# Optimization experiments

Hardware: AMD Instinct MI355X
Metric: run time of the kernel (lower is better)

The kernel has to match this reference:

```python
import jax, jax.numpy as jnp
import numpy as np

B, N, D = 2, 2048, 1536
HEADS, KVH, DQK, DV = 8, 1, 128, 192
G = HEADS // KVH  # query groups per kv head
NP, DP = 512, 128  # pairwise seq len (coarse), pairwise feature dim
SCALE = DQK ** -0.5
CLAMP = 5.0
MOMENTUM = 0.1  # BatchRMSNorm: 1 - 0.9
EPS = 1e-5


def layernorm(x, w, b):
    mu = jnp.mean(x, axis=-1, keepdims=True)
    var = jnp.mean(jnp.square(x - mu), axis=-1, keepdims=True)
    return (x - mu) * jax.lax.rsqrt(var + EPS) * w + b


def setup_inputs() -> dict:
    key = jax.random.key(0)
    ks = jax.random.split(key, 6)
    w = lambda k, shape: jax.random.normal(k, shape, jnp.float32) * 0.02
    return {
        "x": jax.random.normal(ks[0], (B, N, D), jnp.float32),
        "pairwise": jax.random.normal(ks[1], (B, NP, NP, DP), jnp.float32),
        "w_qkv": w(ks[2], (D, HEADS * DQK + KVH * DQK + KVH * DV)),
        "q_w": jnp.ones((DQK,), jnp.float32), "q_b": jnp.zeros((DQK,), jnp.float32),
        "k_w": jnp.ones((DQK,), jnp.float32), "k_b": jnp.zeros((DQK,), jnp.float32),
        "v_w": jnp.ones((DV,), jnp.float32), "v_b": jnp.zeros((DV,), jnp.float32),
        "bias_gamma": jnp.ones((DP,), jnp.float32),
        "bias_beta": jnp.zeros((DP,), jnp.float32),
        "bias_running_var": jnp.ones((DP,), jnp.float32),
        "w_bias": w(ks[3], (DP, HEADS)),
        "w_out": w(ks[4], (HEADS * DV, D)),
        "b_out": jnp.zeros((D,), jnp.float32),
    }


def reference(x, pairwise, w_qkv, q_w, q_b, k_w, k_b, v_w, v_b,
              bias_gamma, bias_beta, bias_running_var, w_bias, w_out, b_out):
    b, n, _ = x.shape
    qkv = x @ w_qkv
    q, k, v = jnp.split(qkv, [HEADS * DQK, HEADS * DQK + KVH * DQK], axis=-1)
    # split heads: q -> b g h n d, k/v -> b h n d
    q = q.reshape(b, n, G, KVH, DQK).transpose(0, 2, 3, 1, 4)
    k = k.reshape(b, n, KVH, DQK).transpose(0, 2, 1, 3)
    v = v.reshape(b, n, KVH, DV).transpose(0, 2, 1, 3)
    q = layernorm(q, q_w, q_b)
    k = layernorm(k, k_w, k_b)
    v = layernorm(v, v_w, v_b)

    sim = jnp.einsum('bghid,bhjd->bghij', q, k) * SCALE

    # BatchRMSNorm (training update of running_var, then normalize)
    flat = pairwise.reshape(-1, DP)
    batch_var = jnp.var(flat, axis=0)  # unbiased=False
    rv = bias_running_var * (1.0 - MOMENTUM) + MOMENTUM * batch_var
    std = jnp.sqrt(rv + EPS)
    normed = pairwise / std * bias_gamma + bias_beta
    bias = jax.nn.gelu(normed, approximate=False) @ w_bias  # b i j (g h)
    bias = bias.reshape(b, NP, NP, G, KVH).transpose(0, 3, 4, 1, 2)  # b g h i j
    r = n // NP  # expand_factor
    bias = jnp.repeat(jnp.repeat(bias, r, axis=-2), r, axis=-1)

    sim = jnp.tanh((sim + bias) / CLAMP) * CLAMP  # softclamp
    attn = jax.nn.softmax(sim, axis=-1)
    out = jnp.einsum('bghij,bhjd->bghid', attn, v)
    out = out.transpose(0, 3, 1, 2, 4).reshape(b, n, HEADS * DV)  # merge heads
    return out @ w_out + b_out
```

## Files before the change

kernel.cpp:

```cpp
#include <hip/hip_runtime.h>
#include <math.h>

typedef _Float16 f16;
typedef unsigned int u32;
typedef __attribute__((ext_vector_type(8))) f16 f16x8;
typedef __attribute__((ext_vector_type(4))) f16 f16x4;
typedef __attribute__((ext_vector_type(4))) float f32x4;
typedef __attribute__((ext_vector_type(16))) float f32x16;

#define DEV static __device__ __forceinline__

#define NB 2
#define SEQ 2048
#define DMODEL 1536
#define NHEADS 8
#define DQK 128
#define DVV 192
#define QKVW 1344
#define SCALEQK 0.08838834764831845f
#define LOG2E 1.4426950408889634f

#define OFF_WQKVT 0ull
#define OFF_WOUTT 4128768ull
#define OFF_QKV   8847360ull
#define OFF_Q     30867456ull
#define OFF_K     39256064ull
#define OFF_V     40304640ull
#define OFF_VT    41877504ull
#define OFF_VSUM  43450368ull
#define OFF_SG    43451392ull
#define OFF_BIASC 43452416ull
#define OFF_AO    60229632ull

DEV float fexp2(float x){
#if __has_builtin(__builtin_amdgcn_exp2f)
  return __builtin_amdgcn_exp2f(x);
#else
  return exp2f(x);
#endif
}
DEV float frcp(float x){
#if __has_builtin(__builtin_amdgcn_rcpf)
  return __builtin_amdgcn_rcpf(x);
#else
  return 1.0f/x;
#endif
}

typedef u32 __attribute__((address_space(1))) u32g;
typedef u32 __attribute__((address_space(3))) u32l;
DEV void g2l16(const void* g, void* l){
  __builtin_amdgcn_global_load_lds((const u32g*)g, (u32l*)l, 16, 0, 0);
}

#define MFMA32(a,b,c) __builtin_amdgcn_mfma_f32_32x32x16_f16(a,b,c,0,0,0)
#define MFMA16(a,b,c) __builtin_amdgcn_mfma_f32_16x16x32_f16(a,b,c,0,0,0)

DEV f32x16 zero16(){
  f32x16 v;
  #pragma unroll
  for (int i=0;i<16;i++) v[i]=0.f;
  return v;
}
DEV f32x4 zero4(){
  f32x4 v;
  #pragma unroll
  for (int i=0;i<4;i++) v[i]=0.f;
  return v;
}
DEV float gelu_f(float x){ return 0.5f*x*(1.f + erff(x*0.70710678118654752440f)); }

__global__ void wtrans(const float* __restrict__ src, f16* __restrict__ dst, int K, int N){
  __shared__ float t[32][33];
  int k0 = blockIdx.x*32, n0 = blockIdx.y*32;
  int tx = threadIdx.x, ty = threadIdx.y;
  #pragma unroll
  for (int i=0;i<4;i++){ int r = ty+8*i; t[r][tx] = src[(size_t)(k0+r)*N + n0+tx]; }
  __syncthreads();
  #pragma unroll
  for (int i=0;i<4;i++){ int r = ty+8*i; dst[(size_t)(n0+r)*K + k0+tx] = (f16)t[tx][r]; }
}

__global__ __launch_bounds__(256,2) void qkv_gemm(const float* __restrict__ X,
                                                  const f16* __restrict__ WT,
                                                  float* __restrict__ qkv){
  __shared__ char lds[49152];
  int nb = blockIdx.x*64, mb = blockIdx.y*128;
  int tid = threadIdx.x;
  int w = tid>>6, lane = tid&63, li = lane&31, h = lane>>5;
  int arow = tid>>4, acq = tid&15;
  int brow = lane>>3, bc = lane&7;
  f32x16 acc[2]; acc[0]=zero16(); acc[1]=zero16();
  f32x4 ar[8];

#define QG_ISSUE_B(buf, kt_) do { \
    char* bd = lds + (buf)*24576 + 16384; \
    _Pragma("unroll") \
    for (int s=0;s<2;s++){ \
      int slot = w*2+s; int nl = slot*8 + brow; int cs = bc ^ (nl&7); \
      g2l16(WT + (size_t)(nb+nl)*DMODEL + (kt_)*64 + cs*8, bd + slot*1024); \
    } } while(0)
#define QG_LOAD_A(kt_) do { \
    _Pragma("unroll") \
    for (int i=0;i<8;i++) \
      ar[i] = *(const f32x4*)(X + (size_t)(mb + arow + 16*i)*DMODEL + (kt_)*64 + acq*4); \
    } while(0)
#define QG_WRITE_A(buf) do { \
    char* ad = lds + (buf)*24576; \
    _Pragma("unroll") \
    for (int i=0;i<8;i++){ \
      int rr = arow + 16*i; int ch = (acq>>1) ^ (rr&7); \
      f16x4 t4; t4[0]=(f16)ar[i][0]; t4[1]=(f16)ar[i][1]; t4[2]=(f16)ar[i][2]; t4[3]=(f16)ar[i][3]; \
      *(f16x4*)(ad + rr*128 + ch*16 + (acq&1)*8) = t4; \
    } } while(0)

  QG_ISSUE_B(0,0); QG_LOAD_A(0); QG_WRITE_A(0);
  __syncthreads();
  for (int kt=0; kt<24; kt++){
    int cur = kt&1;
    if (kt<23){ QG_ISSUE_B(cur^1, kt+1); QG_LOAD_A(kt+1); }
    const char* ad = lds + cur*24576;
    const char* bd = lds + cur*24576 + 16384;
    int ml = w*32 + li;
    #pragma unroll
    for (int ks=0; ks<4; ks++){
      f16x8 af = *(const f16x8*)(ad + ml*128 + (((2*ks+h) ^ (ml&7))*16));
      #pragma unroll
      for (int nf=0; nf<2; nf++){
        int nl = nf*32 + li;
        f16x8 bf = *(const f16x8*)(bd + nl*128 + (((2*ks+h) ^ (nl&7))*16));
        acc[nf] = MFMA32(af, bf, acc[nf]);
      }
    }
    if (kt<23) QG_WRITE_A(cur^1);
    __syncthreads();
  }
  #pragma unroll
  for (int nf=0; nf<2; nf++)
    #pragma unroll
    for (int r=0;r<16;r++){
      int m = mb + w*32 + (r&3) + 8*(r>>2) + 4*h;
      int n = nb + nf*32 + li;
      qkv[(size_t)m*QKVW + n] = acc[nf][r];
    }
#undef QG_ISSUE_B
#undef QG_LOAD_A
#undef QG_WRITE_A
}

__global__ __launch_bounds__(64) void ln_pack(const float* __restrict__ qkv,
    const float* __restrict__ qw, const float* __restrict__ qb,
    const float* __restrict__ kw, const float* __restrict__ kb,
    const float* __restrict__ vw, const float* __restrict__ vb,
    f16* __restrict__ Q, f16* __restrict__ K, f16* __restrict__ V){
  int bid = blockIdx.x;
  int row = bid / 10, seg = bid - row*10;
  int b = row >> 11, n = row & 2047;
  int lane = threadIdx.x;
  const float* base = qkv + (size_t)row*QKVW;
  if (seg < 9){
    int off = seg*128;
    float x0 = base[off+lane], x1 = base[off+64+lane];
    float s = x0+x1;
    #pragma unroll
    for (int d=32; d>=1; d>>=1) s += __shfl_xor(s, d);
    float mu = s*(1.f/128.f);
    float d0 = x0-mu, d1 = x1-mu;
    float vv = d0*d0 + d1*d1;
    #pragma unroll
    for (int d=32; d>=1; d>>=1) vv += __shfl_xor(vv, d);
    float istd = rsqrtf(vv*(1.f/128.f) + 1e-5f);
    const float* W  = (seg<8)? qw : kw;
    const float* Bi = (seg<8)? qb : kb;
    f16* dst = (seg<8) ? (Q + ((size_t)(b*NHEADS+seg)*SEQ + n)*DQK)
                       : (K + ((size_t)(b*SEQ+n))*DQK);
    dst[lane]    = (f16)(d0*istd*W[lane] + Bi[lane]);
    dst[lane+64] = (f16)(d1*istd*W[lane+64] + Bi[lane+64]);
  } else {
    float x0 = base[1152+lane], x1 = base[1152+64+lane], x2 = base[1152+128+lane];
    float s = x0+x1+x2;
    #pragma unroll
    for (int d=32; d>=1; d>>=1) s += __shfl_xor(s, d);
    float mu = s*(1.f/192.f);
    float d0=x0-mu, d1=x1-mu, d2=x2-mu;
    float vv = d0*d0+d1*d1+d2*d2;
    #pragma unroll
    for (int d=32; d>=1; d>>=1) vv += __shfl_xor(vv, d);
    float istd = rsqrtf(vv*(1.f/192.f) + 1e-5f);
    f16* dst = V + (size_t)(b*SEQ+n)*DVV;
    dst[lane]     = (f16)(d0*istd*vw[lane] + vb[lane]);
    dst[lane+64]  = (f16)(d1*istd*vw[lane+64] + vb[lane+64]);
    dst[lane+128] = (f16)(d2*istd*vw[lane+128] + vb[lane+128]);
  }
}

__global__ void vtrans(const f16* __restrict__ V, f16* __restrict__ VT){
  __shared__ f16 t[32][33];
  int b = blockIdx.z; int d0 = blockIdx.x*32; int j0 = blockIdx.y*32;
  int tx = threadIdx.x, ty = threadIdx.y;
  #pragma unroll
  for (int i=0;i<4;i++){ int r = ty+8*i; t[r][tx] = V[((size_t)b*SEQ + j0+r)*DVV + d0+tx]; }
  __syncthreads();
  #pragma unroll
  for (int i=0;i<4;i++){ int r = ty+8*i; VT[((size_t)b*DVV + d0+r)*SEQ + j0+tx] = t[tx][r]; }
}

__global__ __launch_bounds__(256,4) void pvar(const float* __restrict__ pw, float* __restrict__ sums){
  int tid = threadIdx.x;
  int c = tid & 127, hh = tid >> 7;
  float s1 = 0.f, s2 = 0.f;
  const float* p0 = pw + ((size_t)blockIdx.x*512 + hh)*128 + c;
  #pragma unroll 4
  for (int it=0; it<256; it++){
    float v = p0[(size_t)it*256];
    s1 += v; s2 += v*v;
  }
  __shared__ float r1[256], r2[256];
  r1[tid] = s1; r2[tid] = s2;
  __syncthreads();
  if (tid < 128){
    atomicAdd(&sums[c],     r1[tid] + r1[tid+128]);
    atomicAdd(&sums[128+c], r2[tid] + r2[tid+128]);
  }
}

__global__ void finvar(const float* __restrict__ sums, const float* __restrict__ rvar,
                       const float* __restrict__ gamma, const float* __restrict__ beta,
                       float* __restrict__ sg, float* __restrict__ sb){
  int c = threadIdx.x;
  const float Minv = 1.f/524288.f;
  float m = sums[c]*Minv;
  float var = sums[128+c]*Minv - m*m;
  float rv = rvar[c]*0.9f + 0.1f*var;
  float istd = rsqrtf(rv + 1e-5f);
  sg[c] = istd*gamma[c];
  sb[c] = beta[c];
}

__global__ __launch_bounds__(256,2) void bias_gemm(const float* __restrict__ pw,
    const float* __restrict__ sg, const float* __restrict__ sb,
    const float* __restrict__ wb, float* __restrict__ biasc){
  int tid = threadIdx.x;
  int w = tid>>6, lane = tid&63;
  int il = lane&15, kg = lane>>4;
  f16x8 bw[4];
  float sgr[32], sbr[32];
  #pragma unroll
  for (int t=0;t<4;t++)
    #pragma unroll
    for (int e=0;e<8;e++){
      int k = t*32 + kg*8 + e;
      bw[t][e] = (f16)((il<8) ? wb[k*8 + il] : 0.f);
      sgr[t*8+e] = sg[k];
      sbr[t*8+e] = sb[k];
    }
  for (int it=0; it<8; it++){
    int tile = blockIdx.x*4 + w + it*4096;
    size_t rg = (size_t)tile*16 + il;
    f32x4 acc = zero4();
    #pragma unroll
    for (int t=0;t<4;t++){
      const float* sp = pw + rg*128 + t*32 + kg*8;
      f32x4 v0 = *(const f32x4*)sp;
      f32x4 v1 = *(const f32x4*)(sp+4);
      f16x8 af;
      #pragma unroll
      for (int e=0;e<4;e++) af[e]   = (f16)gelu_f(v0[e]*sgr[t*8+e]   + sbr[t*8+e]);
      #pragma unroll
      for (int e=0;e<4;e++) af[4+e] = (f16)gelu_f(v1[e]*sgr[t*8+4+e] + sbr[t*8+4+e]);
      acc = MFMA16(af, bw[t], acc);
    }
    if (il < 8){
      #pragma unroll
      for (int r=0;r<4;r++){
        size_t rr = (size_t)tile*16 + kg*4 + r;
        int bb = (int)(rr >> 18);
        int rem = (int)(rr & 262143);
        int ii = rem >> 9, jj = rem & 511;
        biasc[(((size_t)(bb*8 + il)*512) + ii)*512 + jj] = acc[r];
      }
    }
  }
}

__global__ __launch_bounds__(256,1) void attn(const f16* __restrict__ Q, const f16* __restrict__ K,
                                              const f16* __restrict__ VT, const float* __restrict__ biasc,
                                              f16* __restrict__ AO){
  __shared__ char lds[81920];
  __shared__ float linvb[4][32];
  int bid = blockIdx.x;
  int bg = bid & 15, qt = bid >> 4;
  int b = bg >> 3, g = bg & 7;
  int tid = threadIdx.x;
  int w = tid >> 6, lane = tid & 63;
  int li = lane & 31, h = lane >> 5;

  const f16* Qb = Q  + (size_t)bg*SEQ*DQK;
  const f16* Kb = K  + (size_t)b*SEQ*DQK;
  const f16* Vb = VT + (size_t)b*DVV*SEQ;

  int qrow = qt*128 + w*32 + li;
  f16x8 qf[8];
  #pragma unroll
  for (int ks=0; ks<8; ks++)
    qf[ks] = *(const f16x8*)(Qb + (size_t)qrow*DQK + ks*16 + h*8);

  const float* brow = biasc + ((size_t)bg*512 + (qrow>>2))*512;

  f32x16 oacc[6];
  #pragma unroll
  for (int nf=0;nf<6;nf++) oacc[nf] = zero16();
  float lsum = 0.f;

  int kl_row = lane >> 4, kl_c = lane & 15;
  int vl_row = lane >> 3, vl_c = lane & 7;

#define STAGE(buf, jt_) do { \
    char* kd = lds + (buf)*40960; \
    const f16* ksrc = Kb + (size_t)(jt_)*64*DQK; \
    _Pragma("unroll") \
    for (int s=0;s<4;s++){ \
      int slot = w*4+s; int jr = slot*4 + kl_row; int cs = kl_c ^ (jr&7); \
      g2l16(ksrc + (size_t)jr*DQK + cs*8, kd + slot*1024); \
    } \
    char* vd = lds + (buf)*40960 + 16384; \
    _Pragma("unroll") \
    for (int s=0;s<6;s++){ \
      int slot = w*6+s; int dvr = slot*8 + vl_row; int cs = vl_c ^ (dvr&7); \
      g2l16(Vb + (size_t)dvr*SEQ + (size_t)(jt_)*64 + cs*8, vd + slot*1024); \
    } } while(0)

  STAGE(0, 0);

  const float CS = SCALEQK * (2.f*LOG2E/5.f);
  const float CB = 2.f*LOG2E/5.f;
  const float CP = 5.f*LOG2E;

  for (int jt=0; jt<32; jt++){
    int cur = jt & 1;
    __syncthreads();
    if (jt < 31) STAGE(cur^1, jt+1);
    const char* kb_ = lds + cur*40960;
    const char* vb_ = lds + cur*40960 + 16384;
    #pragma unroll
    for (int sub=0; sub<2; sub++){
      f32x16 sacc = zero16();
      int jr = sub*32 + li;
      #pragma unroll
      for (int ks=0; ks<8; ks++){
        int ck = (2*ks + h) ^ (jr&7);
        f16x8 kf = *(const f16x8*)(kb_ + jr*256 + ck*16);
        sacc = MFMA32(kf, qf[ks], sacc);
      }
      int jb4 = jt*16 + sub*8;
      float bt[4];
      #pragma unroll
      for (int q=0;q<4;q++) bt[q] = brow[jb4 + 2*q + h] * CB;
      float p[16], xp[16];
      #pragma unroll
      for (int r=0;r<16;r++){
        float u2 = sacc[r]*CS + bt[r>>2];
        float E  = fexp2(u2);
        float tn = 1.f - 2.f*frcp(E + 1.f);
        float pr = fexp2(tn * CP);
        p[r] = pr;
        lsum += pr;
      }
      #pragma unroll
      for (int r=0;r<16;r++) xp[r] = __shfl_xor(p[r], 32);
      #pragma unroll
      for (int ks2=0; ks2<2; ks2++){
        f16x8 pa;
        #pragma unroll
        for (int e=0;e<4;e++) pa[e] = (f16)(h ? xp[8*ks2+4+e] : p[8*ks2+e]);
        #pragma unroll
        for (int e=4;e<8;e++) pa[e] = (f16)(h ? p[8*ks2+e]    : xp[8*ks2+e-4]);
        #pragma unroll
        for (int nf=0; nf<6; nf++){
          int dvr = nf*32 + li;
          int cj = (sub*4 + 2*ks2 + h) ^ (dvr&7);
          f16x8 vf = *(const f16x8*)(vb_ + dvr*128 + cj*16);
          oacc[nf] = MFMA32(pa, vf, oacc[nf]);
        }
      }
    }
  }
  float ltot = lsum + __shfl_xor(lsum, 32);
  float linv = 1.f / ltot;
  if (h == 0) linvb[w][li] = linv;
  __syncthreads();
  #pragma unroll
  for (int nf=0; nf<6; nf++)
    #pragma unroll
    for (int r=0;r<16;r++){
      int il = (r&3) + 8*(r>>2) + 4*h;
      float ov = oacc[nf][r] * linvb[w][il];
      int orow = qt*128 + w*32 + il;
      AO[((size_t)(b*SEQ + orow)*NHEADS + g)*DVV + nf*32 + li] = (f16)ov;
    }
#undef STAGE
}

__global__ __launch_bounds__(256,2) void out_gemm(const f16* __restrict__ A, const f16* __restrict__ WT,
                                                  const float* __restrict__ bo, float* __restrict__ out){
  __shared__ char lds[49152];
  int nb = blockIdx.x*64, mb = blockIdx.y*128;
  int tid = threadIdx.x;
  int w = tid>>6, lane = tid&63, li = lane&31, h = lane>>5;
  int srow = lane>>3, sc = lane&7;
  f32x16 acc[2]; acc[0]=zero16(); acc[1]=zero16();

#define OG_STAGE(buf, kt_) do { \
    char* ad = lds + (buf)*24576; \
    _Pragma("unroll") \
    for (int s=0;s<4;s++){ \
      int slot = w*4+s; int mlr = slot*8 + srow; int cs = sc ^ (mlr&7); \
      g2l16(A + (size_t)(mb+mlr)*DMODEL + (kt_)*64 + cs*8, ad + slot*1024); \
    } \
    char* bd = lds + (buf)*24576 + 16384; \
    _Pragma("unroll") \
    for (int s=0;s<2;s++){ \
      int slot = w*2+s; int nl = slot*8 + srow; int cs = sc ^ (nl&7); \
      g2l16(WT + (size_t)(nb+nl)*DMODEL + (kt_)*64 + cs*8, bd + slot*1024); \
    } } while(0)

  OG_STAGE(0,0);
  __syncthreads();
  for (int kt=0; kt<24; kt++){
    int cur = kt&1;
    if (kt<23) OG_STAGE(cur^1, kt+1);
    const char* ad = lds + cur*24576;
    const char* bd = lds + cur*24576 + 16384;
    int ml = w*32 + li;
    #pragma unroll
    for (int ks=0; ks<4; ks++){
      f16x8 af = *(const f16x8*)(ad + ml*128 + (((2*ks+h) ^ (ml&7))*16));
      #pragma unroll
      for (int nf=0; nf<2; nf++){
        int nl = nf*32 + li;
        f16x8 bf = *(const f16x8*)(bd + nl*128 + (((2*ks+h) ^ (nl&7))*16));
        acc[nf] = MFMA32(af, bf, acc[nf]);
      }
    }
    __syncthreads();
  }
  float bo0 = bo[nb+li], bo1 = bo[nb+32+li];
  #pragma unroll
  for (int nf=0; nf<2; nf++)
    #pragma unroll
    for (int r=0;r<16;r++){
      int m = mb + w*32 + (r&3) + 8*(r>>2) + 4*h;
      int n = nb + nf*32 + li;
      out[(size_t)m*DMODEL + n] = acc[nf][r] + (nf ? bo1 : bo0);
    }
#undef OG_STAGE
}

extern "C" void kernel_launch(void* const* d_in, const int* in_sizes, int n_in,
                              void* d_out, int out_size, void* d_ws, size_t ws_size,
                              hipStream_t stream) {
  (void)in_sizes; (void)n_in; (void)out_size; (void)ws_size;
  const float* x        = (const float*)d_in[0];
  const float* pairwise = (const float*)d_in[1];
  const float* w_qkv    = (const float*)d_in[2];
  const float* q_w      = (const float*)d_in[3];
  const float* q_b      = (const float*)d_in[4];
  const float* k_w      = (const float*)d_in[5];
  const float* k_b      = (const float*)d_in[6];
  const float* v_w      = (const float*)d_in[7];
  const float* v_b      = (const float*)d_in[8];
  const float* bgamma   = (const float*)d_in[9];
  const float* bbeta    = (const float*)d_in[10];
  const float* brvar    = (const float*)d_in[11];
  const float* w_bias   = (const float*)d_in[12];
  const float* w_out    = (const float*)d_in[13];
  const float* b_out    = (const float*)d_in[14];
  float* out = (float*)d_out;

  char* ws = (char*)d_ws;
  f16*   wqkvT = (f16*)(ws + OFF_WQKVT);
  f16*   woutT = (f16*)(ws + OFF_WOUTT);
  float* qkvb  = (float*)(ws + OFF_QKV);
  f16*   Qh    = (f16*)(ws + OFF_Q);
  f16*   Kh    = (f16*)(ws + OFF_K);
  f16*   Vh    = (f16*)(ws + OFF_V);
  f16*   VTh   = (f16*)(ws + OFF_VT);
  float* vsum  = (float*)(ws + OFF_VSUM);
  float* sg    = (float*)(ws + OFF_SG);
  float* sb    = sg + 128;
  float* biasc = (float*)(ws + OFF_BIASC);
  f16*   AOh   = (f16*)(ws + OFF_AO);

  (void)hipMemsetAsync(ws + OFF_VSUM, 0, 1024, stream);
  wtrans<<<dim3(48,42), dim3(32,8), 0, stream>>>(w_qkv, wqkvT, 1536, 1344);
  wtrans<<<dim3(48,48), dim3(32,8), 0, stream>>>(w_out, woutT, 1536, 1536);
  qkv_gemm<<<dim3(21,32), 256, 0, stream>>>(x, wqkvT, qkvb);
  ln_pack<<<40960, 64, 0, stream>>>(qkvb, q_w,q_b,k_w,k_b,v_w,v_b, Qh, Kh, Vh);
  vtrans<<<dim3(6,64,2), dim3(32,8), 0, stream>>>(Vh, VTh);
  pvar<<<1024, 256, 0, stream>>>(pairwise, vsum);
  finvar<<<1, 128, 0, stream>>>(vsum, brvar, bgamma, bbeta, sg, sb);
  bias_gemm<<<1024, 256, 0, stream>>>(pairwise, sg, sb, w_bias, biasc);
  attn<<<256, 256, 0, stream>>>(Qh, Kh, VTh, biasc, AOh);
  out_gemm<<<dim3(24,32), 256, 0, stream>>>(AOh, woutT, b_out, out);
}
```

Before: 350.3 us.

## Merge preprocessing kernels into four launches, store bias in fp16, tune attention

Cuts the launch count by combining the two weight transposes into one launch and interleaving the QKV GEMM with the pairwise variance reduction in a single grid. The variance now uses per-block partials instead of atomics, so the memset goes away. LayerNorm is merged with the variance finalisation, and the bias GEMM with the V transpose. The coarse bias is stored as fp16 to halve its traffic in attention. Attention also raises wave priority around its MFMA sections and passes the softmax normaliser by lane shuffle instead of LDS plus a barrier. Risks are lower bias precision, load imbalance in the mixed grids, and possible under-occupancy of the mixed blocks.

```diff
diff --git a/kernel.cpp b/kernel.cpp
--- a/kernel.cpp
+++ b/kernel.cpp
@@ -10,7 +10,6 @@
 
 #define DEV static __device__ __forceinline__
 
-#define NB 2
 #define SEQ 2048
 #define DMODEL 1536
 #define NHEADS 8
@@ -27,10 +26,10 @@
 #define OFF_K     39256064ull
 #define OFF_V     40304640ull
 #define OFF_VT    41877504ull
-#define OFF_VSUM  43450368ull
-#define OFF_SG    43451392ull
-#define OFF_BIASC 43452416ull
-#define OFF_AO    60229632ull
+#define OFF_PART  43450368ull
+#define OFF_SG    43712512ull
+#define OFF_BIASC 43713536ull
+#define OFF_AO    52102144ull
 
 DEV float fexp2(float x){
 #if __has_builtin(__builtin_amdgcn_exp2f)
@@ -70,23 +69,25 @@
 }
 DEV float gelu_f(float x){ return 0.5f*x*(1.f + erff(x*0.70710678118654752440f)); }
 
-__global__ void wtrans(const float* __restrict__ src, f16* __restrict__ dst, int K, int N){
+__global__ __launch_bounds__(256) void k1_wtrans(const float* __restrict__ wq, f16* __restrict__ wqT,
+                                                 const float* __restrict__ wo, f16* __restrict__ woT){
   __shared__ float t[32][33];
-  int k0 = blockIdx.x*32, n0 = blockIdx.y*32;
-  int tx = threadIdx.x, ty = threadIdx.y;
+  int bid = blockIdx.x, tid = threadIdx.x;
+  int tx = tid & 31, ty = tid >> 5;
+  const float* src; f16* dst; int N, x, y;
+  if (bid < 2016){ src = wq; dst = wqT; N = 1344; x = bid % 48; y = bid / 48; }
+  else { int b2 = bid - 2016; src = wo; dst = woT; N = 1536; x = b2 % 48; y = b2 / 48; }
+  int k0 = x*32, n0 = y*32;
   #pragma unroll
   for (int i=0;i<4;i++){ int r = ty+8*i; t[r][tx] = src[(size_t)(k0+r)*N + n0+tx]; }
   __syncthreads();
   #pragma unroll
-  for (int i=0;i<4;i++){ int r = ty+8*i; dst[(size_t)(n0+r)*K + k0+tx] = (f16)t[tx][r]; }
-}
-
-__global__ __launch_bounds__(256,2) void qkv_gemm(const float* __restrict__ X,
-                                                  const f16* __restrict__ WT,
-                                                  float* __restrict__ qkv){
-  __shared__ char lds[49152];
-  int nb = blockIdx.x*64, mb = blockIdx.y*128;
-  int tid = threadIdx.x;
+  for (int i=0;i<4;i++){ int r = ty+8*i; dst[(size_t)(n0+r)*1536 + k0+tx] = (f16)t[tx][r]; }
+}
+
+DEV void qkv_body(const float* __restrict__ X, const f16* __restrict__ WT,
+                  float* __restrict__ qkv, char* lds, int bx, int by, int tid){
+  int nb = bx*64, mb = by*128;
   int w = tid>>6, lane = tid&63, li = lane&31, h = lane>>5;
   int arow = tid>>4, acq = tid&15;
   int brow = lane>>3, bc = lane&7;
@@ -148,15 +149,47 @@
 #undef QG_WRITE_A
 }
 
-__global__ __launch_bounds__(64) void ln_pack(const float* __restrict__ qkv,
+DEV void pvar_body(const float* __restrict__ pw, float* __restrict__ partials,
+                   char* smem, int id, int tid){
+  int c = tid & 127, hh = tid >> 7;
+  float s1 = 0.f, s2 = 0.f;
+  const float* p0 = pw + ((size_t)id*2048 + hh)*128 + c;
+  #pragma unroll 8
+  for (int it=0; it<1024; it++){
+    float v = p0[(size_t)it*256];
+    s1 += v; s2 += v*v;
+  }
+  float* r1 = (float*)smem; float* r2 = r1 + 256;
+  r1[tid] = s1; r2[tid] = s2;
+  __syncthreads();
+  if (tid < 128){
+    partials[(size_t)id*256 + tid]       = r1[tid] + r1[tid+128];
+    partials[(size_t)id*256 + 128 + tid] = r2[tid] + r2[tid+128];
+  }
+}
+
+__global__ __launch_bounds__(256,2) void k2_qkv_pvar(const float* __restrict__ X,
+    const f16* __restrict__ WT, float* __restrict__ qkv,
+    const float* __restrict__ pw, float* __restrict__ partials){
+  __shared__ char smem[49152];
+  int bid = blockIdx.x, tid = threadIdx.x;
+  if (bid < 512){
+    if ((bid & 1) == 0){ int qid = bid>>1; qkv_body(X, WT, qkv, smem, qid%21, qid/21, tid); }
+    else               { pvar_body(pw, partials, smem, bid>>1, tid); }
+  } else {
+    int qid = 256 + (bid - 512);
+    qkv_body(X, WT, qkv, smem, qid%21, qid/21, tid);
+  }
+}
+
+DEV void ln_unit(const float* __restrict__ qkv,
     const float* __restrict__ qw, const float* __restrict__ qb,
     const float* __restrict__ kw, const float* __restrict__ kb,
     const float* __restrict__ vw, const float* __restrict__ vb,
-    f16* __restrict__ Q, f16* __restrict__ K, f16* __restrict__ V){
-  int bid = blockIdx.x;
-  int row = bid / 10, seg = bid - row*10;
+    f16* __restrict__ Q, f16* __restrict__ K, f16* __restrict__ V,
+    int unit, int lane){
+  int row = unit / 10, seg = unit - row*10;
   int b = row >> 11, n = row & 2047;
-  int lane = threadIdx.x;
   const float* base = qkv + (size_t)row*QKVW;
   if (seg < 9){
     int off = seg*128;
@@ -194,53 +227,40 @@
   }
 }
 
-__global__ void vtrans(const f16* __restrict__ V, f16* __restrict__ VT){
-  __shared__ f16 t[32][33];
-  int b = blockIdx.z; int d0 = blockIdx.x*32; int j0 = blockIdx.y*32;
-  int tx = threadIdx.x, ty = threadIdx.y;
-  #pragma unroll
-  for (int i=0;i<4;i++){ int r = ty+8*i; t[r][tx] = V[((size_t)b*SEQ + j0+r)*DVV + d0+tx]; }
-  __syncthreads();
-  #pragma unroll
-  for (int i=0;i<4;i++){ int r = ty+8*i; VT[((size_t)b*DVV + d0+r)*SEQ + j0+tx] = t[tx][r]; }
-}
-
-__global__ __launch_bounds__(256,4) void pvar(const float* __restrict__ pw, float* __restrict__ sums){
-  int tid = threadIdx.x;
-  int c = tid & 127, hh = tid >> 7;
-  float s1 = 0.f, s2 = 0.f;
-  const float* p0 = pw + ((size_t)blockIdx.x*512 + hh)*128 + c;
-  #pragma unroll 4
-  for (int it=0; it<256; it++){
-    float v = p0[(size_t)it*256];
-    s1 += v; s2 += v*v;
-  }
-  __shared__ float r1[256], r2[256];
-  r1[tid] = s1; r2[tid] = s2;
-  __syncthreads();
-  if (tid < 128){
-    atomicAdd(&sums[c],     r1[tid] + r1[tid+128]);
-    atomicAdd(&sums[128+c], r2[tid] + r2[tid+128]);
-  }
-}
-
-__global__ void finvar(const float* __restrict__ sums, const float* __restrict__ rvar,
-                       const float* __restrict__ gamma, const float* __restrict__ beta,
-                       float* __restrict__ sg, float* __restrict__ sb){
-  int c = threadIdx.x;
-  const float Minv = 1.f/524288.f;
-  float m = sums[c]*Minv;
-  float var = sums[128+c]*Minv - m*m;
-  float rv = rvar[c]*0.9f + 0.1f*var;
-  float istd = rsqrtf(rv + 1e-5f);
-  sg[c] = istd*gamma[c];
-  sb[c] = beta[c];
-}
-
-__global__ __launch_bounds__(256,2) void bias_gemm(const float* __restrict__ pw,
+__global__ __launch_bounds__(256,4) void k3_ln_finvar(const float* __restrict__ qkv,
+    const float* __restrict__ qw, const float* __restrict__ qb,
+    const float* __restrict__ kw, const float* __restrict__ kb,
+    const float* __restrict__ vw, const float* __restrict__ vb,
+    f16* __restrict__ Q, f16* __restrict__ K, f16* __restrict__ V,
+    const float* __restrict__ partials, const float* __restrict__ rvar,
+    const float* __restrict__ gamma, const float* __restrict__ beta,
+    float* __restrict__ sg, float* __restrict__ sb){
+  __shared__ float sh[256];
+  int bid = blockIdx.x, tid = threadIdx.x;
+  if (bid < 10240){
+    ln_unit(qkv, qw,qb,kw,kb,vw,vb, Q,K,V, bid*4 + (tid>>6), tid&63);
+  } else {
+    int c = tid & 127, wh = tid >> 7;
+    float acc = 0.f;
+    #pragma unroll 4
+    for (int i=0;i<256;i++) acc += partials[i*256 + wh*128 + c];
+    sh[tid] = acc;
+    __syncthreads();
+    if (tid < 128){
+      float s1 = sh[tid], s2 = sh[tid+128];
+      const float Minv = 1.f/524288.f;
+      float m = s1*Minv;
+      float var = s2*Minv - m*m;
+      float rv = rvar[tid]*0.9f + 0.1f*var;
+      sg[tid] = rsqrtf(rv + 1e-5f)*gamma[tid];
+      sb[tid] = beta[tid];
+    }
+  }
+}
+
+DEV void bias_body(const float* __restrict__ pw,
     const float* __restrict__ sg, const float* __restrict__ sb,
-    const float* __restrict__ wb, float* __restrict__ biasc){
-  int tid = threadIdx.x;
+    const float* __restrict__ wb, f16* __restrict__ biasc, int bias_id, int tid){
   int w = tid>>6, lane = tid&63;
   int il = lane&15, kg = lane>>4;
   f16x8 bw[4];
@@ -255,7 +275,7 @@
       sbr[t*8+e] = sb[k];
     }
   for (int it=0; it<8; it++){
-    int tile = blockIdx.x*4 + w + it*4096;
+    int tile = bias_id*4 + w + it*4096;
     size_t rg = (size_t)tile*16 + il;
     f32x4 acc = zero4();
     #pragma unroll
@@ -277,17 +297,42 @@
         int bb = (int)(rr >> 18);
         int rem = (int)(rr & 262143);
         int ii = rem >> 9, jj = rem & 511;
-        biasc[(((size_t)(bb*8 + il)*512) + ii)*512 + jj] = acc[r];
-      }
-    }
+        biasc[(((size_t)(bb*8 + il)*512) + ii)*512 + jj] = (f16)acc[r];
+      }
+    }
+  }
+}
+
+DEV void vtrans_body(const f16* __restrict__ V, f16* __restrict__ VT,
+                     f16 (*t)[33], int id, int tid){
+  int b = id / 384, rem = id - b*384;
+  int d0 = (rem % 6)*32, j0 = (rem / 6)*32;
+  int tx = tid & 31, ty = tid >> 5;
+  #pragma unroll
+  for (int i=0;i<4;i++){ int r = ty+8*i; t[r][tx] = V[((size_t)b*SEQ + j0+r)*DVV + d0+tx]; }
+  __syncthreads();
+  #pragma unroll
+  for (int i=0;i<4;i++){ int r = ty+8*i; VT[((size_t)b*DVV + d0+r)*SEQ + j0+tx] = t[tx][r]; }
+}
+
+__global__ __launch_bounds__(256,2) void k4_bias_vtrans(const float* __restrict__ pw,
+    const float* __restrict__ sg, const float* __restrict__ sb,
+    const float* __restrict__ wb, f16* __restrict__ biasc,
+    const f16* __restrict__ V, f16* __restrict__ VT){
+  __shared__ f16 tt[32][33];
+  int bid = blockIdx.x, tid = threadIdx.x;
+  if (bid < 1536){
+    if (bid & 1) bias_body(pw, sg, sb, wb, biasc, bid>>1, tid);
+    else         vtrans_body(V, VT, tt, bid>>1, tid);
+  } else {
+    bias_body(pw, sg, sb, wb, biasc, 768 + (bid - 1536), tid);
   }
 }
 
 __global__ __launch_bounds__(256,1) void attn(const f16* __restrict__ Q, const f16* __restrict__ K,
-                                              const f16* __restrict__ VT, const float* __restrict__ biasc,
+                                              const f16* __restrict__ VT, const f16* __restrict__ biasc,
                                               f16* __restrict__ AO){
   __shared__ char lds[81920];
-  __shared__ float linvb[4][32];
   int bid = blockIdx.x;
   int bg = bid & 15, qt = bid >> 4;
   int b = bg >> 3, g = bg & 7;
@@ -305,7 +350,7 @@
   for (int ks=0; ks<8; ks++)
     qf[ks] = *(const f16x8*)(Qb + (size_t)qrow*DQK + ks*16 + h*8);
 
-  const float* brow = biasc + ((size_t)bg*512 + (qrow>>2))*512;
+  const f16* brow = biasc + ((size_t)bg*512 + (qrow>>2))*512;
 
   f32x16 oacc[6];
   #pragma unroll
@@ -346,16 +391,22 @@
     for (int sub=0; sub<2; sub++){
       f32x16 sacc = zero16();
       int jr = sub*32 + li;
+      __builtin_amdgcn_s_setprio(1);
       #pragma unroll
       for (int ks=0; ks<8; ks++){
         int ck = (2*ks + h) ^ (jr&7);
         f16x8 kf = *(const f16x8*)(kb_ + jr*256 + ck*16);
         sacc = MFMA32(kf, qf[ks], sacc);
       }
+      __builtin_amdgcn_s_setprio(0);
       int jb4 = jt*16 + sub*8;
+      f16x8 bv = *(const f16x8*)(brow + jb4);
       float bt[4];
       #pragma unroll
-      for (int q=0;q<4;q++) bt[q] = brow[jb4 + 2*q + h] * CB;
+      for (int q=0;q<4;q++){
+        float b0 = (float)bv[2*q], b1 = (float)bv[2*q+1];
+        bt[q] = (h ? b1 : b0) * CB;
+      }
       float p[16], xp[16];
       #pragma unroll
       for (int r=0;r<16;r++){
@@ -368,6 +419,7 @@
       }
       #pragma unroll
       for (int r=0;r<16;r++) xp[r] = __shfl_xor(p[r], 32);
+      __builtin_amdgcn_s_setprio(1);
       #pragma unroll
       for (int ks2=0; ks2<2; ks2++){
         f16x8 pa;
@@ -383,18 +435,17 @@
           oacc[nf] = MFMA32(pa, vf, oacc[nf]);
         }
       }
+      __builtin_amdgcn_s_setprio(0);
     }
   }
   float ltot = lsum + __shfl_xor(lsum, 32);
   float linv = 1.f / ltot;
-  if (h == 0) linvb[w][li] = linv;
-  __syncthreads();
   #pragma unroll
   for (int nf=0; nf<6; nf++)
     #pragma unroll
     for (int r=0;r<16;r++){
       int il = (r&3) + 8*(r>>2) + 4*h;
-      float ov = oacc[nf][r] * linvb[w][il];
+      float ov = oacc[nf][r] * __shfl(linv, il);
       int orow = qt*128 + w*32 + il;
       AO[((size_t)(b*SEQ + orow)*NHEADS + g)*DVV + nf*32 + li] = (f16)ov;
     }
@@ -485,21 +536,17 @@
   f16*   Kh    = (f16*)(ws + OFF_K);
   f16*   Vh    = (f16*)(ws + OFF_V);
   f16*   VTh   = (f16*)(ws + OFF_VT);
-  float* vsum  = (float*)(ws + OFF_VSUM);
+  float* part  = (float*)(ws + OFF_PART);
   float* sg    = (float*)(ws + OFF_SG);
   float* sb    = sg + 128;
-  float* biasc = (float*)(ws + OFF_BIASC);
+  f16*   biasc = (f16*)(ws + OFF_BIASC);
   f16*   AOh   = (f16*)(ws + OFF_AO);
 
-  (void)hipMemsetAsync(ws + OFF_VSUM, 0, 1024, stream);
-  wtrans<<<dim3(48,42), dim3(32,8), 0, stream>>>(w_qkv, wqkvT, 1536, 1344);
-  wtrans<<<dim3(48,48), dim3(32,8), 0, stream>>>(w_out, woutT, 1536, 1536);
-  qkv_gemm<<<dim3(21,32), 256, 0, stream>>>(x, wqkvT, qkvb);
-  ln_pack<<<40960, 64, 0, stream>>>(qkvb, q_w,q_b,k_w,k_b,v_w,v_b, Qh, Kh, Vh);
-  vtrans<<<dim3(6,64,2), dim3(32,8), 0, stream>>>(Vh, VTh);
-  pvar<<<1024, 256, 0, stream>>>(pairwise, vsum);
-  finvar<<<1, 128, 0, stream>>>(vsum, brvar, bgamma, bbeta, sg, sb);
-  bias_gemm<<<1024, 256, 0, stream>>>(pairwise, sg, sb, w_bias, biasc);
+  k1_wtrans<<<4320, 256, 0, stream>>>(w_qkv, wqkvT, w_out, woutT);
+  k2_qkv_pvar<<<928, 256, 0, stream>>>(x, wqkvT, qkvb, pairwise, part);
+  k3_ln_finvar<<<10241, 256, 0, stream>>>(qkvb, q_w,q_b,k_w,k_b,v_w,v_b, Qh, Kh, Vh,
+                                          part, brvar, bgamma, bbeta, sg, sb);
+  k4_bias_vtrans<<<1792, 256, 0, stream>>>(pairwise, sg, sb, w_bias, biasc, Vh, VTh);
   attn<<<256, 256, 0, stream>>>(Qh, Kh, VTh, biasc, AOh);
   out_gemm<<<dim3(24,32), 256, 0, stream>>>(AOh, woutT, b_out, out);
 }
```

Result: slower. 384.9 us (+9.9%).
